# Kernel optimization log

Measured on AMD Instinct MI355X. Metric: run time of the kernel, lower is better.

## Reference

```python
import jax, jax.numpy as jnp
import numpy as np

MAX_LOGIT = 30.0
COV_WEIGHT = 1.0


def setup_inputs() -> dict:
    key = jax.random.key(0)
    ks = jax.random.split(key, 8)
    B, T, S, H = 8, 100, 400, 256
    sc = 1.0 / np.sqrt(H)
    return {
        "decoder_outputs": jax.random.normal(ks[0], (B, T, H), jnp.float32),
        "encoder_outputs": jax.random.normal(ks[1], (B, S, H), jnp.float32),
        "src_mask": jnp.zeros((B, S), dtype=bool),
        "W_h": jax.random.normal(ks[2], (H, H), jnp.float32) * sc,
        "W_s": jax.random.normal(ks[3], (H, H), jnp.float32) * sc,
        "w_c": jax.random.normal(ks[4], (H,), jnp.float32) * sc,  # Linear(1,H) weight
        "v": jax.random.normal(ks[5], (H,), jnp.float32) * sc,    # Linear(H,1) weight
        "b_attn": jnp.zeros((H,), jnp.float32),
    }


def reference(decoder_outputs, encoder_outputs, src_mask, W_h, W_s, w_c, v, b_attn):
    B, T, H = decoder_outputs.shape
    S = encoder_outputs.shape[1]
    neg_inf = jnp.float32(-jnp.inf)

    Wh = jnp.einsum('bsh,hk->bsk', encoder_outputs, W_h)   # [B,S,H]
    Ws = jnp.einsum('bth,hk->btk', decoder_outputs, W_s)   # [B,T,H]
    # E_base: [B,T,S,H]
    E_base = Wh[:, None, :, :] + Ws[:, :, None, :] + b_attn

    def logits(x):
        e = jnp.einsum('btsh,h->bts', jnp.tanh(x), v)
        e = jnp.clip(e, -MAX_LOGIT, MAX_LOGIT)
        return jnp.where(src_mask[:, None, :], neg_inf, e)

    A_prelim = jax.nn.softmax(logits(E_base), axis=-1)      # [B,T,S]
    cum = jnp.cumsum(A_prelim, axis=1)
    cov_shifted = jnp.concatenate(
        [jnp.zeros((B, 1, S), A_prelim.dtype), cum[:, :-1, :]], axis=1)  # [B,T,S]

    # W_c applied to scalar coverage: outer product with w_c -> [B,T,S,H]
    E_final = logits(E_base + cov_shifted[..., None] * w_c)
    A_final = jax.nn.softmax(E_final, axis=-1)              # [B,T,S]

    context = jnp.einsum('bts,bsh->bth', A_final, encoder_outputs)
    cov_loss = (COV_WEIGHT * jnp.sum(jnp.minimum(A_final, cov_shifted), axis=-1).mean())[None]
    return context, A_final, cov_loss
```

## Files before the change

kernel.cpp:

```cpp
#include <hip/hip_runtime.h>
#include <math.h>

#define B_ 8
#define T_ 100
#define S_ 400
#define H_ 256
#define BT_ (B_ * T_)
#define MAXL 30.0f
#define K_EXP 2.885390081777927f

#define AF_OFF (BT_ * H_)
#define LOSS_OFF (BT_ * H_ + BT_ * S_)

#define EWHT_OFF 0
#define EWSB_OFF (B_ * H_ * S_)
#define ACOV_OFF (EWSB_OFF + BT_ * H_)

__device__ __forceinline__ float wave_sum(float p) {
#pragma unroll
    for (int off = 32; off; off >>= 1) p += __shfl_xor(p, off, 64);
    return p;
}

__device__ __forceinline__ float wave_max(float p) {
#pragma unroll
    for (int off = 32; off; off >>= 1) p = fmaxf(p, __shfl_xor(p, off, 64));
    return p;
}

#define ROWS 8
__global__ __launch_bounds__(256) void k_gemm(
    const float* __restrict__ dec, const float* __restrict__ enc,
    const float* __restrict__ W_h, const float* __restrict__ W_s,
    const float* __restrict__ b_attn,
    float* __restrict__ EWhT, float* __restrict__ EWsb) {
    const int tid = threadIdx.x;
    const int blk = blockIdx.x;
    const int NB_ENC = (B_ * S_) / ROWS;

    float acc[ROWS];
#pragma unroll
    for (int r = 0; r < ROWS; ++r) acc[r] = 0.f;

    if (blk < NB_ENC) {
        const int r0 = blk * ROWS;
        const int b = r0 / S_, s0 = r0 - b * S_;
        const float* in = enc + (size_t)r0 * H_;
        const float* Wp = W_h + tid;
#pragma unroll 4
        for (int h = 0; h < H_; ++h) {
            float w = Wp[(size_t)h * H_];
#pragma unroll
            for (int r = 0; r < ROWS; ++r)
                acc[r] = fmaf(in[r * H_ + h], w, acc[r]);
        }
        float* o = EWhT + ((size_t)b * H_ + tid) * S_ + s0;
#pragma unroll
        for (int r = 0; r < ROWS; ++r)
            o[r] = __builtin_amdgcn_exp2f(K_EXP * acc[r]);
    } else {
        const int bt0 = (blk - NB_ENC) * ROWS;
        const float* in = dec + (size_t)bt0 * H_;
        const float* Wp = W_s + tid;
        const float bias = b_attn[tid];
#pragma unroll 4
        for (int h = 0; h < H_; ++h) {
            float w = Wp[(size_t)h * H_];
#pragma unroll
            for (int r = 0; r < ROWS; ++r)
                acc[r] = fmaf(in[r * H_ + h], w, acc[r]);
        }
#pragma unroll
        for (int r = 0; r < ROWS; ++r)
            EWsb[(size_t)(bt0 + r) * H_ + tid] =
                __builtin_amdgcn_exp2f(K_EXP * (acc[r] + bias));
    }
}

__global__ __launch_bounds__(512) void k_prelim(
    const float* __restrict__ EWhT, const float* __restrict__ EWsb,
    const float* __restrict__ v,
    const unsigned char* __restrict__ mask,
    float* __restrict__ A) {
    __shared__ float red[32];
    const int blk = blockIdx.x;
    const int b = blk & 7;
    const int tp = blk >> 3;
    const int bt0 = b * T_ + 2 * tp;
    const int tid = threadIdx.x;
    const int lane = tid & 63;
    const int wid = tid >> 6;
    const int s = tid;
    const bool act = (s < S_);

    const float4 vv4 = *reinterpret_cast<const float4*>(v + 4 * lane);
    const float sumv = wave_sum((vv4.x + vv4.y) + (vv4.z + vv4.w));

    const float* E0 = EWsb + (size_t)bt0 * H_;
    const float* E1 = E0 + H_;
    float acc0 = 0.f, acc1 = 0.f;
    if (act) {
        const float* ecol = EWhT + (size_t)b * H_ * S_ + s;
#pragma unroll 8
        for (int h = 0; h < H_; ++h) {
            float Ew = ecol[(size_t)h * S_];
            float vh = v[h];
            float r0 = __builtin_amdgcn_rcpf(fmaf(Ew, E0[h], 1.0f));
            float r1 = __builtin_amdgcn_rcpf(fmaf(Ew, E1[h], 1.0f));
            acc0 = fmaf(r0, vh, acc0);
            acc1 = fmaf(r1, vh, acc1);
        }
    }

    float e0 = -INFINITY, e1 = -INFINITY;
    if (act) {
        e0 = fminf(fmaxf(sumv - 2.f * acc0, -MAXL), MAXL);
        e1 = fminf(fmaxf(sumv - 2.f * acc1, -MAXL), MAXL);
        if (mask[(size_t)b * S_ + s]) { e0 = -INFINITY; e1 = -INFINITY; }
    }

    float mx0 = wave_max(e0);
    float mx1 = wave_max(e1);
    if (lane == 0) { red[wid] = mx0; red[8 + wid] = mx1; }
    __syncthreads();
    mx0 = fmaxf(fmaxf(fmaxf(red[0], red[1]), fmaxf(red[2], red[3])),
                fmaxf(fmaxf(red[4], red[5]), fmaxf(red[6], red[7])));
    mx1 = fmaxf(fmaxf(fmaxf(red[8], red[9]), fmaxf(red[10], red[11])),
                fmaxf(fmaxf(red[12], red[13]), fmaxf(red[14], red[15])));

    float p0 = act ? __expf(e0 - mx0) : 0.f;
    float p1 = act ? __expf(e1 - mx1) : 0.f;
    float sm0 = wave_sum(p0);
    float sm1 = wave_sum(p1);
    if (lane == 0) { red[16 + wid] = sm0; red[24 + wid] = sm1; }
    __syncthreads();
    sm0 = ((red[16] + red[17]) + (red[18] + red[19])) +
          ((red[20] + red[21]) + (red[22] + red[23]));
    sm1 = ((red[24] + red[25]) + (red[26] + red[27])) +
          ((red[28] + red[29]) + (red[30] + red[31]));

    if (act) {
        A[(size_t)bt0 * S_ + s] = p0 * __builtin_amdgcn_rcpf(sm0);
        A[(size_t)(bt0 + 1) * S_ + s] = p1 * __builtin_amdgcn_rcpf(sm1);
    }
}

__global__ __launch_bounds__(64) void k_cumsum(float* __restrict__ A,
                                               float* __restrict__ out) {
    const int idx = blockIdx.x * 64 + threadIdx.x;
    if (idx == 0) out[LOSS_OFF] = 0.f;
    if (idx >= B_ * S_) return;
    const int b = idx / S_;
    const int s = idx - b * S_;
    float* col = A + (size_t)b * T_ * S_ + s;
    float run = 0.f;
#pragma unroll 10
    for (int t = 0; t < T_; ++t) {
        float a = col[(size_t)t * S_];
        col[(size_t)t * S_] = run;
        run += a;
    }
}

__global__ __launch_bounds__(512) void k_final(
    const float* __restrict__ EWhT, const float* __restrict__ EWsb,
    const float* __restrict__ v, const float* __restrict__ w_c,
    const float* __restrict__ cov,
    const unsigned char* __restrict__ mask,
    const float* __restrict__ enc,
    float* __restrict__ out) {
    __shared__ float e0_lds[S_], e1_lds[S_];
    __shared__ float ctx0[H_], ctx1[H_];
    __shared__ float red[32];
    const int blk = blockIdx.x;
    const int b = blk & 7;
    const int tp = blk >> 3;
    const int bt0 = b * T_ + 2 * tp;
    const int tid = threadIdx.x;
    const int lane = tid & 63;
    const int wid = tid >> 6;
    const int s = tid;
    const bool act = (s < S_);

    const float4 vv4 = *reinterpret_cast<const float4*>(v + 4 * lane);
    const float sumv = wave_sum((vv4.x + vv4.y) + (vv4.z + vv4.w));

    float c0 = 0.f, c1 = 0.f;
    if (act) {
        c0 = cov[(size_t)bt0 * S_ + s];
        c1 = cov[(size_t)(bt0 + 1) * S_ + s];
    }
    const float ck0 = K_EXP * c0, ck1 = K_EXP * c1;

    const float* E0 = EWsb + (size_t)bt0 * H_;
    const float* E1 = E0 + H_;
    float acc0 = 0.f, acc1 = 0.f;
    if (act) {
        const float* ecol = EWhT + (size_t)b * H_ * S_ + s;
#pragma unroll 8
        for (int h = 0; h < H_; ++h) {
            float Ew = ecol[(size_t)h * S_];
            float wch = w_c[h];
            float vh = v[h];
            float Ec0 = __builtin_amdgcn_exp2f(ck0 * wch);
            float Ec1 = __builtin_amdgcn_exp2f(ck1 * wch);
            float r0 = __builtin_amdgcn_rcpf(fmaf(Ew * E0[h], Ec0, 1.0f));
            float r1 = __builtin_amdgcn_rcpf(fmaf(Ew * E1[h], Ec1, 1.0f));
            acc0 = fmaf(r0, vh, acc0);
            acc1 = fmaf(r1, vh, acc1);
        }
    }

    float e0 = -INFINITY, e1 = -INFINITY;
    if (act) {
        e0 = fminf(fmaxf(sumv - 2.f * acc0, -MAXL), MAXL);
        e1 = fminf(fmaxf(sumv - 2.f * acc1, -MAXL), MAXL);
        if (mask[(size_t)b * S_ + s]) { e0 = -INFINITY; e1 = -INFINITY; }
    }

    float mx0 = wave_max(e0);
    float mx1 = wave_max(e1);
    if (lane == 0) { red[wid] = mx0; red[8 + wid] = mx1; }
    __syncthreads();
    mx0 = fmaxf(fmaxf(fmaxf(red[0], red[1]), fmaxf(red[2], red[3])),
                fmaxf(fmaxf(red[4], red[5]), fmaxf(red[6], red[7])));
    mx1 = fmaxf(fmaxf(fmaxf(red[8], red[9]), fmaxf(red[10], red[11])),
                fmaxf(fmaxf(red[12], red[13]), fmaxf(red[14], red[15])));

    float p0 = act ? __expf(e0 - mx0) : 0.f;
    float p1 = act ? __expf(e1 - mx1) : 0.f;
    float sm0 = wave_sum(p0);
    float sm1 = wave_sum(p1);
    if (lane == 0) { red[16 + wid] = sm0; red[24 + wid] = sm1; }
    __syncthreads();
    sm0 = ((red[16] + red[17]) + (red[18] + red[19])) +
          ((red[20] + red[21]) + (red[22] + red[23]));
    sm1 = ((red[24] + red[25]) + (red[26] + red[27])) +
          ((red[28] + red[29]) + (red[30] + red[31]));

    const float a0 = act ? p0 * __builtin_amdgcn_rcpf(sm0) : 0.f;
    const float a1 = act ? p1 * __builtin_amdgcn_rcpf(sm1) : 0.f;

    float lp = act ? (fminf(a0, c0) + fminf(a1, c1)) : 0.f;
    lp = wave_sum(lp);
    if (lane == 0) red[wid] = lp;

    if (act) {
        e0_lds[s] = a0;
        e1_lds[s] = a1;
        out[AF_OFF + (size_t)bt0 * S_ + s] = a0;
        out[AF_OFF + (size_t)(bt0 + 1) * S_ + s] = a1;
    }
    __syncthreads();

    if (tid == 0) {
        float tot = ((red[0] + red[1]) + (red[2] + red[3])) +
                    ((red[4] + red[5]) + (red[6] + red[7]));
        atomicAdd(out + LOSS_OFF, tot * (1.0f / (B_ * T_)));
    }

    const int h = tid & (H_ - 1);
    const int half = tid >> 8;
    const int sb = half * (S_ / 2);
    const float* eb = enc + ((size_t)b * S_ + sb) * H_ + h;
    float q00 = 0.f, q01 = 0.f, q02 = 0.f, q03 = 0.f;
    float q10 = 0.f, q11 = 0.f, q12 = 0.f, q13 = 0.f;
#pragma unroll 5
    for (int j = 0; j < S_ / 2; j += 4) {
        float w0 = eb[(size_t)j * H_];
        float w1 = eb[(size_t)(j + 1) * H_];
        float w2 = eb[(size_t)(j + 2) * H_];
        float w3 = eb[(size_t)(j + 3) * H_];
        q00 = fmaf(e0_lds[sb + j], w0, q00);
        q10 = fmaf(e1_lds[sb + j], w0, q10);
        q01 = fmaf(e0_lds[sb + j + 1], w1, q01);
        q11 = fmaf(e1_lds[sb + j + 1], w1, q11);
        q02 = fmaf(e0_lds[sb + j + 2], w2, q02);
        q12 = fmaf(e1_lds[sb + j + 2], w2, q12);
        q03 = fmaf(e0_lds[sb + j + 3], w3, q03);
        q13 = fmaf(e1_lds[sb + j + 3], w3, q13);
    }
    const float r0 = (q00 + q01) + (q02 + q03);
    const float r1 = (q10 + q11) + (q12 + q13);
    if (half == 0) { ctx0[h] = r0; ctx1[h] = r1; }
    __syncthreads();
    if (half == 1) {
        out[(size_t)bt0 * H_ + h] = ctx0[h] + r0;
        out[(size_t)(bt0 + 1) * H_ + h] = ctx1[h] + r1;
    }
}

extern "C" void kernel_launch(void* const* d_in, const int* in_sizes, int n_in,
                              void* d_out, int out_size, void* d_ws, size_t ws_size,
                              hipStream_t stream) {
    const float* dec = (const float*)d_in[0];
    const float* enc = (const float*)d_in[1];
    const unsigned char* mask = (const unsigned char*)d_in[2];
    const float* W_h = (const float*)d_in[3];
    const float* W_s = (const float*)d_in[4];
    const float* w_c = (const float*)d_in[5];
    const float* v = (const float*)d_in[6];
    const float* b_attn = (const float*)d_in[7];

    float* out = (float*)d_out;
    float* ws = (float*)d_ws;
    float* EWhT = ws + EWHT_OFF;
    float* EWsb = ws + EWSB_OFF;
    float* Acov = ws + ACOV_OFF;

    const int nb_gemm = (B_ * S_) / ROWS + BT_ / ROWS;
    const int nb_pair = B_ * (T_ / 2);
    k_gemm<<<nb_gemm, 256, 0, stream>>>(dec, enc, W_h, W_s, b_attn, EWhT, EWsb);
    k_prelim<<<nb_pair, 512, 0, stream>>>(EWhT, EWsb, v, mask, Acov);
    k_cumsum<<<(B_ * S_ + 63) / 64, 64, 0, stream>>>(Acov, out);
    k_final<<<nb_pair, 512, 0, stream>>>(EWhT, EWsb, v, w_c, Acov, mask, enc, out);
}
```

Before: 162.2 us.

## Interleave encoder exponent table by 4 and merge reciprocals in prelim

The encoder exp(2*Wh) table is stored with four consecutive H values interleaved per sequence position, so the prelim and final kernels fetch one float4 per thread instead of four strided scalars. In the prelim kernel the four reciprocals per group are folded into a single reciprocal of the product of denominators, with a combined numerator. This cuts transcendental instruction count and load instructions. The product of four (1+x) terms can overflow or lose accuracy when the exponentials are large, which is a numerical risk.

```diff
diff --git a/kernel.cpp b/kernel.cpp
--- a/kernel.cpp
+++ b/kernel.cpp
@@ -5,6 +5,7 @@
 #define T_ 100
 #define S_ 400
 #define H_ 256
+#define HQ_ (H_ / 4)
 #define BT_ (B_ * T_)
 #define MAXL 30.0f
 #define K_EXP 2.885390081777927f
@@ -33,7 +34,7 @@
     const float* __restrict__ dec, const float* __restrict__ enc,
     const float* __restrict__ W_h, const float* __restrict__ W_s,
     const float* __restrict__ b_attn,
-    float* __restrict__ EWhT, float* __restrict__ EWsb) {
+    float* __restrict__ EWhT4, float* __restrict__ EWsb) {
     const int tid = threadIdx.x;
     const int blk = blockIdx.x;
     const int NB_ENC = (B_ * S_) / ROWS;
@@ -54,10 +55,10 @@
             for (int r = 0; r < ROWS; ++r)
                 acc[r] = fmaf(in[r * H_ + h], w, acc[r]);
         }
-        float* o = EWhT + ((size_t)b * H_ + tid) * S_ + s0;
+        float* o = EWhT4 + (((size_t)b * HQ_ + (tid >> 2)) * S_ + s0) * 4 + (tid & 3);
 #pragma unroll
         for (int r = 0; r < ROWS; ++r)
-            o[r] = __builtin_amdgcn_exp2f(K_EXP * acc[r]);
+            o[r * 4] = __builtin_amdgcn_exp2f(K_EXP * acc[r]);
     } else {
         const int bt0 = (blk - NB_ENC) * ROWS;
         const float* in = dec + (size_t)bt0 * H_;
@@ -78,7 +79,7 @@
 }
 
 __global__ __launch_bounds__(512) void k_prelim(
-    const float* __restrict__ EWhT, const float* __restrict__ EWsb,
+    const float* __restrict__ EWhT4, const float* __restrict__ EWsb,
     const float* __restrict__ v,
     const unsigned char* __restrict__ mask,
     float* __restrict__ A) {
@@ -100,15 +101,33 @@
     const float* E1 = E0 + H_;
     float acc0 = 0.f, acc1 = 0.f;
     if (act) {
-        const float* ecol = EWhT + (size_t)b * H_ * S_ + s;
-#pragma unroll 8
-        for (int h = 0; h < H_; ++h) {
-            float Ew = ecol[(size_t)h * S_];
-            float vh = v[h];
-            float r0 = __builtin_amdgcn_rcpf(fmaf(Ew, E0[h], 1.0f));
-            float r1 = __builtin_amdgcn_rcpf(fmaf(Ew, E1[h], 1.0f));
-            acc0 = fmaf(r0, vh, acc0);
-            acc1 = fmaf(r1, vh, acc1);
+        const float4* eq = reinterpret_cast<const float4*>(
+                               EWhT4 + (size_t)b * HQ_ * S_ * 4) + s;
+#pragma unroll 4
+        for (int hq = 0; hq < HQ_; ++hq) {
+            const float4 Ew = eq[(size_t)hq * S_];
+            const int h = 4 * hq;
+            const float v0 = v[h], v1 = v[h + 1], v2 = v[h + 2], v3 = v[h + 3];
+            {
+                float p0 = fmaf(Ew.x, E0[h], 1.f);
+                float p1 = fmaf(Ew.y, E0[h + 1], 1.f);
+                float p2 = fmaf(Ew.z, E0[h + 2], 1.f);
+                float p3 = fmaf(Ew.w, E0[h + 3], 1.f);
+                float p01 = p0 * p1, p23 = p2 * p3;
+                float num = fmaf(fmaf(v0, p1, v1 * p0), p23,
+                                 fmaf(v2, p3, v3 * p2) * p01);
+                acc0 = fmaf(num, __builtin_amdgcn_rcpf(p01 * p23), acc0);
+            }
+            {
+                float p0 = fmaf(Ew.x, E1[h], 1.f);
+                float p1 = fmaf(Ew.y, E1[h + 1], 1.f);
+                float p2 = fmaf(Ew.z, E1[h + 2], 1.f);
+                float p3 = fmaf(Ew.w, E1[h + 3], 1.f);
+                float p01 = p0 * p1, p23 = p2 * p3;
+                float num = fmaf(fmaf(v0, p1, v1 * p0), p23,
+                                 fmaf(v2, p3, v3 * p2) * p01);
+                acc1 = fmaf(num, __builtin_amdgcn_rcpf(p01 * p23), acc1);
+            }
         }
     }
 
@@ -163,7 +182,7 @@
 }
 
 __global__ __launch_bounds__(512) void k_final(
-    const float* __restrict__ EWhT, const float* __restrict__ EWsb,
+    const float* __restrict__ EWhT4, const float* __restrict__ EWsb,
     const float* __restrict__ v, const float* __restrict__ w_c,
     const float* __restrict__ cov,
     const unsigned char* __restrict__ mask,
@@ -196,18 +215,24 @@
     const float* E1 = E0 + H_;
     float acc0 = 0.f, acc1 = 0.f;
     if (act) {
-        const float* ecol = EWhT + (size_t)b * H_ * S_ + s;
-#pragma unroll 8
-        for (int h = 0; h < H_; ++h) {
-            float Ew = ecol[(size_t)h * S_];
-            float wch = w_c[h];
-            float vh = v[h];
-            float Ec0 = __builtin_amdgcn_exp2f(ck0 * wch);
-            float Ec1 = __builtin_amdgcn_exp2f(ck1 * wch);
-            float r0 = __builtin_amdgcn_rcpf(fmaf(Ew * E0[h], Ec0, 1.0f));
-            float r1 = __builtin_amdgcn_rcpf(fmaf(Ew * E1[h], Ec1, 1.0f));
-            acc0 = fmaf(r0, vh, acc0);
-            acc1 = fmaf(r1, vh, acc1);
+        const float4* eq = reinterpret_cast<const float4*>(
+                               EWhT4 + (size_t)b * HQ_ * S_ * 4) + s;
+#pragma unroll 4
+        for (int hq = 0; hq < HQ_; ++hq) {
+            const float4 Ew = eq[(size_t)hq * S_];
+            const int h = 4 * hq;
+#pragma unroll
+            for (int j = 0; j < 4; ++j) {
+                const float Ewj = j == 0 ? Ew.x : j == 1 ? Ew.y : j == 2 ? Ew.z : Ew.w;
+                const float wch = w_c[h + j];
+                const float vh = v[h + j];
+                float Ec0 = __builtin_amdgcn_exp2f(ck0 * wch);
+                float Ec1 = __builtin_amdgcn_exp2f(ck1 * wch);
+                float r0 = __builtin_amdgcn_rcpf(fmaf(Ewj * E0[h + j], Ec0, 1.0f));
+                float r1 = __builtin_amdgcn_rcpf(fmaf(Ewj * E1[h + j], Ec1, 1.0f));
+                acc0 = fmaf(r0, vh, acc0);
+                acc1 = fmaf(r1, vh, acc1);
+            }
         }
     }
 
@@ -304,14 +329,14 @@
 
     float* out = (float*)d_out;
     float* ws = (float*)d_ws;
-    float* EWhT = ws + EWHT_OFF;
+    float* EWhT4 = ws + EWHT_OFF;
     float* EWsb = ws + EWSB_OFF;
     float* Acov = ws + ACOV_OFF;
 
     const int nb_gemm = (B_ * S_) / ROWS + BT_ / ROWS;
     const int nb_pair = B_ * (T_ / 2);
-    k_gemm<<<nb_gemm, 256, 0, stream>>>(dec, enc, W_h, W_s, b_attn, EWhT, EWsb);
-    k_prelim<<<nb_pair, 512, 0, stream>>>(EWhT, EWsb, v, mask, Acov);
+    k_gemm<<<nb_gemm, 256, 0, stream>>>(dec, enc, W_h, W_s, b_attn, EWhT4, EWsb);
+    k_prelim<<<nb_pair, 512, 0, stream>>>(EWhT4, EWsb, v, mask, Acov);
     k_cumsum<<<(B_ * S_ + 63) / 64, 64, 0, stream>>>(Acov, out);
-    k_final<<<nb_pair, 512, 0, stream>>>(EWhT, EWsb, v, w_c, Acov, mask, enc, out);
-}
+    k_final<<<nb_pair, 512, 0, stream>>>(EWhT4, EWsb, v, w_c, Acov, mask, enc, out);
+}
```

Measured after the change: 155.4 us. -4.2%, faster.
